# Performance work log

Hardware: AMD Instinct MI355X
Metric: run time of the kernel (lower is better)

Reference implementation:

```python
import jax, jax.numpy as jnp
from jax import lax
import numpy as np

N_FEATURES = 64
B, H, W = 2, 64, 64
EPS = 1e-12  # F.normalize default eps


def setup_inputs() -> dict:
    key = jax.random.key(0)
    ks = jax.random.split(key, 10)
    L = N_FEATURES
    s = 0.02
    return {
        "x": jax.random.normal(ks[0], (B, L, H, W), dtype=jnp.float32),
        "conv1_w": jax.random.normal(ks[1], (L, L, 3, 3), dtype=jnp.float32) * s,
        "conv1_b": jax.random.normal(ks[2], (L,), dtype=jnp.float32) * s,
        "conv2_w": jax.random.normal(ks[3], (L, L, 3, 3), dtype=jnp.float32) * s,
        "conv2_b": jax.random.normal(ks[4], (L,), dtype=jnp.float32) * s,
        "wq": jax.random.normal(ks[5], (L, L), dtype=jnp.float32) * s,
        "wk": jax.random.normal(ks[6], (L, L), dtype=jnp.float32) * s,
        "wv": jax.random.normal(ks[7], (L, L), dtype=jnp.float32) * s,
        "wo": jax.random.normal(ks[8], (L, L), dtype=jnp.float32) * s,
        "bo": jax.random.normal(ks[9], (L,), dtype=jnp.float32) * s,
    }


def _conv3x3(h, w, b):
    y = lax.conv_general_dilated(
        h, w, window_strides=(1, 1), padding=((1, 1), (1, 1)),
        dimension_numbers=("NCHW", "OIHW", "NCHW"))
    return y + b[None, :, None, None]


def _l2norm(a):
    return a / jnp.maximum(jnp.linalg.norm(a, axis=-1, keepdims=True), EPS)


def reference(x, conv1_w, conv1_b, conv2_w, conv2_b, wq, wk, wv, wo, bo):
    # embedding: conv3x3 -> relu -> conv3x3
    h = _conv3x3(x, conv1_w, conv1_b)
    h = jax.nn.relu(h)
    h = _conv3x3(h, conv2_w, conv2_b)  # [B, L, H, W]
    b, l, hh, ww = h.shape
    t = h.reshape(b, l, hh * ww).transpose(0, 2, 1)  # [B, HW, L]
    q = _l2norm(t @ wq.T)  # [B, HW, L]
    k = _l2norm(t @ wk.T)
    v = t @ wv.T
    # per-token rank-1 outer product scores: [B, HW, L, L]
    scores = q[..., :, None] * k[..., None, :]
    p = jax.nn.softmax(scores, axis=-1)
    out = jnp.einsum("bncd,bnd->bnc", p, v)  # [B, HW, L]
    out = out @ wo.T + bo
    out = out.transpose(0, 2, 1).reshape(b, l, hh, ww)
    return out + h
```

## Files before the change

### kernel.cpp

```cpp
#include <hip/hip_runtime.h>
#include <hip/hip_bf16.h>


#define IMG 262144

using frag_ab = __attribute__((ext_vector_type(8))) short;
using frag_cd = __attribute__((ext_vector_type(4))) float;
typedef unsigned u32x4 __attribute__((ext_vector_type(4)));
typedef float    f32x2 __attribute__((ext_vector_type(2)));
typedef float    f32x4 __attribute__((ext_vector_type(4)));

static __device__ inline unsigned short f2bf(float f) {
    unsigned u = __float_as_uint(f);
    return (unsigned short)((u + 0x7FFFu + ((u >> 16) & 1u)) >> 16);
}
static __device__ inline float bflo(unsigned p) { return __uint_as_float(p << 16); }
static __device__ inline float bfhi(unsigned p) { return __uint_as_float(p & 0xFFFF0000u); }

#if __has_builtin(__builtin_amdgcn_fdot2_f32_bf16)
typedef __bf16 bf16x2 __attribute__((ext_vector_type(2)));
static __device__ inline float dot2bf(unsigned a, unsigned b, float c) {
    union U { unsigned u; bf16x2 v; };
    U ua, ub; ua.u = a; ub.u = b;
    return __builtin_amdgcn_fdot2_f32_bf16(ua.v, ub.v, c, false);
}
#else
static __device__ inline float dot2bf(unsigned a, unsigned b, float c) {
    return fmaf(bflo(a), bflo(b), fmaf(bfhi(a), bfhi(b), c));
}
#endif

#if __has_builtin(__builtin_amdgcn_exp2f)
#define EXP2F(x) __builtin_amdgcn_exp2f(x)
#else
#define EXP2F(x) __expf(0.6931471805599453f * (x))
#endif

__global__ __launch_bounds__(256) void prep_w(
    const float* __restrict__ w1, const float* __restrict__ w2,
    const float* __restrict__ wq, const float* __restrict__ wk,
    const float* __restrict__ wv, const float* __restrict__ wo,
    unsigned short* __restrict__ wt1, unsigned short* __restrict__ wt2,
    unsigned* __restrict__ wp)
{
    int i = blockIdx.x * 256 + threadIdx.x;
    if (i < 73728) {
        int mat = i >= 36864;
        int j = i - mat * 36864;
        int tap = j >> 12;
        int oc  = (j >> 6) & 63;
        int ic  = j & 63;
        const float* w = mat ? w2 : w1;
        (mat ? wt2 : wt1)[j] = f2bf(w[(oc * 64 + ic) * 9 + tap]);
    } else {
        int a = i - 73728;
        int mat = a >> 11;
        int r = a & 2047;
        int c = r >> 5, dp = r & 31;
        const float* w = (mat == 0) ? wq : (mat == 1) ? wk : (mat == 2) ? wv : wo;
        unsigned val = (unsigned)f2bf(w[c * 64 + 2 * dp]) |
                       ((unsigned)f2bf(w[c * 64 + 2 * dp + 1]) << 16);
        wp[mat * 2048 + c * 32 + (((dp >> 2) ^ (c & 7)) << 2) + (dp & 3)] = val;
    }
}

__global__ __launch_bounds__(256, 2) void fused_k(
    const float* __restrict__ x,
    const unsigned short* __restrict__ wt1, const unsigned short* __restrict__ wt2,
    const float* __restrict__ b1, const float* __restrict__ b2,
    const unsigned* __restrict__ wp, const float* __restrict__ bo,
    float* __restrict__ out)
{
    __shared__ __align__(16) unsigned       w_lds[6144];
    __shared__ __align__(16) unsigned short xt[5 * 20 * 72];
    __shared__ __align__(16) unsigned short r1[54 * 72];
    __shared__ __align__(16) float          t_lds[16 * 66];
    __shared__ __align__(16) unsigned       tp[16 * 32];
    __shared__ __align__(16) f32x2          kv[8 * 64];
    __shared__ __align__(16) unsigned short o_l[8 * 64];

    const int tid  = threadIdx.x;
    const int b    = blockIdx.x >> 8;
    const int y    = (blockIdx.x >> 2) & 63;
    const int x0   = (blockIdx.x & 3) * 16;
    const int wv_  = tid >> 6;
    const int lane = tid & 63;
    const int m    = lane & 15;
    const int q    = lane >> 4;
    const int oc0  = wv_ * 16;

    frag_ab A1[9][2], A2[9][2];
    #pragma unroll
    for (int t = 0; t < 9; ++t)
        #pragma unroll
        for (int s = 0; s < 2; ++s) {
            A1[t][s] = *(const frag_ab*)&wt1[(t * 64 + oc0 + m) * 64 + s * 32 + q * 8];
            A2[t][s] = *(const frag_ab*)&wt2[(t * 64 + oc0 + m) * 64 + s * 32 + q * 8];
        }

    #pragma unroll
    for (int j = 0; j < 6; ++j)
        ((u32x4*)w_lds)[j * 256 + tid] = ((const u32x4*)wp)[j * 256 + tid];

    {
        const int xl  = tid & 15;
        const int sub = tid >> 4;
        #pragma unroll
        for (int i = 0; i < 20; ++i) {
            int pair = i * 16 + sub;
            int row = pair >> 6, ic = pair & 63;
            int yy = y - 2 + row;
            int yc = min(max(yy, 0), 63);
            float f = x[((b * 64 + ic) * 64 + yc) * 64 + x0 + xl];
            unsigned short v = f2bf(f);
            if (yy != yc) v = 0;
            xt[(row * 20 + xl + 2) * 72 + ic] = v;
        }
        #pragma unroll
        for (int j = 0; j < 5; ++j) {
            int e = j * 256 + tid;
            int col = e & 3, pair = e >> 2;
            int row = pair >> 6, ic = pair & 63;
            int xsl = (col < 2) ? col : col + 16;
            int gx = x0 - 2 + xsl;
            int gxc = min(max(gx, 0), 63);
            int yy = y - 2 + row;
            int yc = min(max(yy, 0), 63);
            float f = x[((b * 64 + ic) * 64 + yc) * 64 + gxc];
            unsigned short v = f2bf(f);
            if (yy != yc || gx != gxc) v = 0;
            xt[(row * 20 + xsl) * 72 + ic] = v;
        }
    }
    __syncthreads();

    int pb[4], rn_[4], xs_[4];
    bool nv[4];
    #pragma unroll
    for (int nt = 0; nt < 4; ++nt) {
        int n  = nt * 16 + m;
        int nc = min(n, 53);
        int rr = nc / 18, xx = nc - rr * 18;
        rn_[nt] = rr; xs_[nt] = xx; nv[nt] = (n < 54);
        pb[nt] = (rr * 20 + xx) * 72 + q * 8;
    }
    frag_cd acc1[4];
    #pragma unroll
    for (int i = 0; i < 4; ++i) acc1[i] = (frag_cd){0.f, 0.f, 0.f, 0.f};

    #pragma unroll
    for (int ky = 0; ky < 3; ++ky)
        #pragma unroll
        for (int kx = 0; kx < 3; ++kx)
            #pragma unroll
            for (int s = 0; s < 2; ++s) {
                frag_ab a = A1[ky * 3 + kx][s];
                int off = (ky * 20 + kx) * 72 + s * 32;
                #pragma unroll
                for (int nt = 0; nt < 4; ++nt)
                    acc1[nt] = __builtin_amdgcn_mfma_f32_16x16x32_bf16(
                        a, *(const frag_ab*)&xt[pb[nt] + off], acc1[nt], 0, 0, 0);
            }

    {
        frag_cd b1f = *(const frag_cd*)&b1[oc0 + q * 4];
        #pragma unroll
        for (int nt = 0; nt < 4; ++nt) {
            if (!nv[nt]) continue;
            int n = nt * 16 + m;
            int gy = y - 1 + rn_[nt];
            int gx = x0 - 1 + xs_[nt];
            bool oob = (gy < 0) | (gy > 63) | (gx < 0) | (gx > 63);
            #pragma unroll
            for (int r = 0; r < 4; ++r) {
                float v = fmaxf(acc1[nt][r] + b1f[r], 0.f);
                r1[n * 72 + oc0 + q * 4 + r] = oob ? (unsigned short)0 : f2bf(v);
            }
        }
    }
    __syncthreads();

    frag_cd acc2 = (frag_cd){0.f, 0.f, 0.f, 0.f};
    #pragma unroll
    for (int ky = 0; ky < 3; ++ky)
        #pragma unroll
        for (int kx = 0; kx < 3; ++kx)
            #pragma unroll
            for (int s = 0; s < 2; ++s)
                acc2 = __builtin_amdgcn_mfma_f32_16x16x32_bf16(
                    A2[ky * 3 + kx][s],
                    *(const frag_ab*)&r1[(ky * 18 + m + kx) * 72 + s * 32 + q * 8],
                    acc2, 0, 0, 0);

    {
        frag_cd b2f = *(const frag_cd*)&b2[oc0 + q * 4];
        float hv[4];
        #pragma unroll
        for (int r = 0; r < 4; ++r) {
            hv[r] = acc2[r] + b2f[r];
            t_lds[m * 66 + oc0 + q * 4 + r] = hv[r];
        }
        int dpb = (oc0 >> 1) + q * 2;
        tp[m * 32 + dpb + 0] = (unsigned)f2bf(hv[0]) | ((unsigned)f2bf(hv[1]) << 16);
        tp[m * 32 + dpb + 1] = (unsigned)f2bf(hv[2]) | ((unsigned)f2bf(hv[3]) << 16);
    }
    __syncthreads();

    const float bo_c = bo[lane];
    const int c7 = lane & 7;
    const unsigned* wop = wp + 6144;
    const int ra_ = wv_ * 2, rb_ = ra_ + 1;

    #pragma unroll
    for (int it = 0; it < 2; ++it) {
        const int ta = wv_ * 4 + it * 2, tb = ta + 1;

        float qa = 0.f, ka = 0.f, va = 0.f, qb = 0.f, kb = 0.f, vb = 0.f;
        #pragma unroll
        for (int dp4 = 0; dp4 < 8; ++dp4) {
            int chunk = ((dp4 ^ c7) << 2);
            u32x4 pq = *(const u32x4*)&w_lds[lane * 32 + chunk];
            u32x4 pk = *(const u32x4*)&w_lds[2048 + lane * 32 + chunk];
            u32x4 pv = *(const u32x4*)&w_lds[4096 + lane * 32 + chunk];
            u32x4 tpa = *(const u32x4*)&tp[ta * 32 + dp4 * 4];
            u32x4 tpb = *(const u32x4*)&tp[tb * 32 + dp4 * 4];
            #pragma unroll
            for (int j = 0; j < 4; ++j) {
                qa = dot2bf(pq[j], tpa[j], qa);
                ka = dot2bf(pk[j], tpa[j], ka);
                va = dot2bf(pv[j], tpa[j], va);
                qb = dot2bf(pq[j], tpb[j], qb);
                kb = dot2bf(pk[j], tpb[j], kb);
                vb = dot2bf(pv[j], tpb[j], vb);
            }
        }

        float nqa = qa * qa, nka = ka * ka, nqb = qb * qb, nkb = kb * kb;
        #pragma unroll
        for (int s = 32; s > 0; s >>= 1) {
            nqa += __shfl_xor(nqa, s);
            nka += __shfl_xor(nka, s);
            nqb += __shfl_xor(nqb, s);
            nkb += __shfl_xor(nkb, s);
        }
        qa = qa / fmaxf(sqrtf(nqa), 1e-12f) * 1.44269504f;
        ka = ka / fmaxf(sqrtf(nka), 1e-12f);
        qb = qb / fmaxf(sqrtf(nqb), 1e-12f) * 1.44269504f;
        kb = kb / fmaxf(sqrtf(nkb), 1e-12f);

        kv[ra_ * 64 + lane] = (f32x2){ka, va};
        kv[rb_ * 64 + lane] = (f32x2){kb, vb};

        float dena = 0.f, numa = 0.f, denb = 0.f, numb = 0.f;
        #pragma unroll 8
        for (int d2 = 0; d2 < 32; ++d2) {
            f32x4 A_ = *(const f32x4*)&kv[ra_ * 64 + d2 * 2];
            f32x4 B_ = *(const f32x4*)&kv[rb_ * 64 + d2 * 2];
            float e0 = EXP2F(qa * A_[0]); dena += e0; numa = fmaf(e0, A_[1], numa);
            float e1 = EXP2F(qa * A_[2]); dena += e1; numa = fmaf(e1, A_[3], numa);
            float e2 = EXP2F(qb * B_[0]); denb += e2; numb = fmaf(e2, B_[1], numb);
            float e3 = EXP2F(qb * B_[2]); denb += e3; numb = fmaf(e3, B_[3], numb);
        }
        float oa = numa / dena, ob = numb / denb;
        o_l[ra_ * 64 + lane] = f2bf(oa);
        o_l[rb_ * 64 + lane] = f2bf(ob);

        float res_a = t_lds[ta * 66 + lane];
        float res_b = t_lds[tb * 66 + lane];
        float oa2 = bo_c, ob2 = bo_c;
        #pragma unroll
        for (int dp4 = 0; dp4 < 8; ++dp4) {
            u32x4 pw  = *(const u32x4*)&wop[lane * 32 + ((dp4 ^ c7) << 2)];
            u32x4 opa = *(const u32x4*)&o_l[ra_ * 64 + dp4 * 8];
            u32x4 opb = *(const u32x4*)&o_l[rb_ * 64 + dp4 * 8];
            #pragma unroll
            for (int j = 0; j < 4; ++j) {
                oa2 = dot2bf(pw[j], opa[j], oa2);
                ob2 = dot2bf(pw[j], opb[j], ob2);
            }
        }
        t_lds[ta * 66 + lane] = oa2 + res_a;
        t_lds[tb * 66 + lane] = ob2 + res_b;
    }
    __syncthreads();

    {
        int c = tid >> 2, xg = tid & 3;
        f32x4 o4;
        #pragma unroll
        for (int j = 0; j < 4; ++j) o4[j] = t_lds[(xg * 4 + j) * 66 + c];
        *(f32x4*)&out[((b * 64 + c) * 64 + y) * 64 + x0 + xg * 4] = o4;
    }
}

extern "C" void kernel_launch(void* const* d_in, const int* in_sizes, int n_in,
                              void* d_out, int out_size, void* d_ws, size_t ws_size,
                              hipStream_t stream) {
    const float* x  = (const float*)d_in[0];
    const float* w1 = (const float*)d_in[1];
    const float* b1 = (const float*)d_in[2];
    const float* w2 = (const float*)d_in[3];
    const float* b2 = (const float*)d_in[4];
    const float* wq = (const float*)d_in[5];
    const float* wk = (const float*)d_in[6];
    const float* wv = (const float*)d_in[7];
    const float* wo = (const float*)d_in[8];
    const float* bo = (const float*)d_in[9];
    float* out = (float*)d_out;

    unsigned*       wpp = (unsigned*)d_ws;
    unsigned short* wt1 = (unsigned short*)((char*)d_ws + 32768);
    unsigned short* wt2 = wt1 + 36864;

    prep_w<<<320, 256, 0, stream>>>(w1, w2, wq, wk, wv, wo, wt1, wt2, wpp);
    fused_k<<<512, 256, 0, stream>>>(x, wt1, wt2, b1, b2, wpp, bo, out);
}
```

Before: 96.88 us.

## Drop weight LDS staging, load fragments coalesced, defer conv2 weights, process four tokens

Weights are repacked so each wave's MFMA A-fragments and the q/k/v/o projection rows load as contiguous coalesced vectors from global memory (L2). The 24KB w_lds staging buffer and its copy are removed. Loading of the conv2 weight fragments is moved until after conv1, which shortens their register lifetime. The occupancy hint is raised from 2 to 3 blocks per CU. The attention stage now handles four tokens per wave in one pass instead of two iterations of two, raising ILP, at the cost of more live registers and of projection weights being read from global/L2 instead of LDS.

```diff
diff --git a/kernel.cpp b/kernel.cpp
--- a/kernel.cpp
+++ b/kernel.cpp
@@ -51,7 +51,10 @@
         int oc  = (j >> 6) & 63;
         int ic  = j & 63;
         const float* w = mat ? w2 : w1;
-        (mat ? wt2 : wt1)[j] = f2bf(w[(oc * 64 + ic) * 9 + tap]);
+        int g = oc >> 4, m = oc & 15;
+        int s = ic >> 5, q = (ic >> 3) & 3, e = ic & 7;
+        int dst = ((((tap * 4 + g) * 2 + s) * 4 + q) * 16 + m) * 8 + e;
+        (mat ? wt2 : wt1)[dst] = f2bf(w[(oc * 64 + ic) * 9 + tap]);
     } else {
         int a = i - 73728;
         int mat = a >> 11;
@@ -60,24 +63,23 @@
         const float* w = (mat == 0) ? wq : (mat == 1) ? wk : (mat == 2) ? wv : wo;
         unsigned val = (unsigned)f2bf(w[c * 64 + 2 * dp]) |
                        ((unsigned)f2bf(w[c * 64 + 2 * dp + 1]) << 16);
-        wp[mat * 2048 + c * 32 + (((dp >> 2) ^ (c & 7)) << 2) + (dp & 3)] = val;
-    }
-}
-
-__global__ __launch_bounds__(256, 2) void fused_k(
+        wp[((mat * 8 + (dp >> 2)) * 64 + c) * 4 + (dp & 3)] = val;
+    }
+}
+
+__global__ __launch_bounds__(256, 3) void fused_k(
     const float* __restrict__ x,
     const unsigned short* __restrict__ wt1, const unsigned short* __restrict__ wt2,
     const float* __restrict__ b1, const float* __restrict__ b2,
     const unsigned* __restrict__ wp, const float* __restrict__ bo,
     float* __restrict__ out)
 {
-    __shared__ __align__(16) unsigned       w_lds[6144];
     __shared__ __align__(16) unsigned short xt[5 * 20 * 72];
     __shared__ __align__(16) unsigned short r1[54 * 72];
     __shared__ __align__(16) float          t_lds[16 * 66];
     __shared__ __align__(16) unsigned       tp[16 * 32];
-    __shared__ __align__(16) f32x2          kv[8 * 64];
-    __shared__ __align__(16) unsigned short o_l[8 * 64];
+    __shared__ __align__(16) f32x2          kv[16 * 64];
+    __shared__ __align__(16) unsigned short o_l[16 * 64];
 
     const int tid  = threadIdx.x;
     const int b    = blockIdx.x >> 8;
@@ -89,18 +91,12 @@
     const int q    = lane >> 4;
     const int oc0  = wv_ * 16;
 
-    frag_ab A1[9][2], A2[9][2];
+    frag_ab A1[9][2];
     #pragma unroll
     for (int t = 0; t < 9; ++t)
         #pragma unroll
-        for (int s = 0; s < 2; ++s) {
-            A1[t][s] = *(const frag_ab*)&wt1[(t * 64 + oc0 + m) * 64 + s * 32 + q * 8];
-            A2[t][s] = *(const frag_ab*)&wt2[(t * 64 + oc0 + m) * 64 + s * 32 + q * 8];
-        }
-
-    #pragma unroll
-    for (int j = 0; j < 6; ++j)
-        ((u32x4*)w_lds)[j * 256 + tid] = ((const u32x4*)wp)[j * 256 + tid];
+        for (int s = 0; s < 2; ++s)
+            A1[t][s] = *(const frag_ab*)&wt1[(((t * 4 + wv_) * 2 + s) * 64 + lane) * 8];
 
     {
         const int xl  = tid & 15;
@@ -162,6 +158,13 @@
                         a, *(const frag_ab*)&xt[pb[nt] + off], acc1[nt], 0, 0, 0);
             }
 
+    frag_ab A2[9][2];
+    #pragma unroll
+    for (int t = 0; t < 9; ++t)
+        #pragma unroll
+        for (int s = 0; s < 2; ++s)
+            A2[t][s] = *(const frag_ab*)&wt2[(((t * 4 + wv_) * 2 + s) * 64 + lane) * 8];
+
     {
         frag_cd b1f = *(const frag_cd*)&b1[oc0 + q * 4];
         #pragma unroll
@@ -207,81 +210,77 @@
     __syncthreads();
 
     const float bo_c = bo[lane];
-    const int c7 = lane & 7;
-    const unsigned* wop = wp + 6144;
-    const int ra_ = wv_ * 2, rb_ = ra_ + 1;
-
-    #pragma unroll
-    for (int it = 0; it < 2; ++it) {
-        const int ta = wv_ * 4 + it * 2, tb = ta + 1;
-
-        float qa = 0.f, ka = 0.f, va = 0.f, qb = 0.f, kb = 0.f, vb = 0.f;
-        #pragma unroll
-        for (int dp4 = 0; dp4 < 8; ++dp4) {
-            int chunk = ((dp4 ^ c7) << 2);
-            u32x4 pq = *(const u32x4*)&w_lds[lane * 32 + chunk];
-            u32x4 pk = *(const u32x4*)&w_lds[2048 + lane * 32 + chunk];
-            u32x4 pv = *(const u32x4*)&w_lds[4096 + lane * 32 + chunk];
-            u32x4 tpa = *(const u32x4*)&tp[ta * 32 + dp4 * 4];
-            u32x4 tpb = *(const u32x4*)&tp[tb * 32 + dp4 * 4];
+    const int t0_ = wv_ * 4;
+
+    float qq[4] = {0,0,0,0}, kk[4] = {0,0,0,0}, vv[4] = {0,0,0,0};
+    #pragma unroll
+    for (int dp4 = 0; dp4 < 8; ++dp4) {
+        u32x4 pq = *(const u32x4*)&wp[(dp4 * 64 + lane) * 4];
+        u32x4 pk = *(const u32x4*)&wp[((8 + dp4) * 64 + lane) * 4];
+        u32x4 pv = *(const u32x4*)&wp[((16 + dp4) * 64 + lane) * 4];
+        #pragma unroll
+        for (int i = 0; i < 4; ++i) {
+            u32x4 tpv = *(const u32x4*)&tp[(t0_ + i) * 32 + dp4 * 4];
             #pragma unroll
             for (int j = 0; j < 4; ++j) {
-                qa = dot2bf(pq[j], tpa[j], qa);
-                ka = dot2bf(pk[j], tpa[j], ka);
-                va = dot2bf(pv[j], tpa[j], va);
-                qb = dot2bf(pq[j], tpb[j], qb);
-                kb = dot2bf(pk[j], tpb[j], kb);
-                vb = dot2bf(pv[j], tpb[j], vb);
+                qq[i] = dot2bf(pq[j], tpv[j], qq[i]);
+                kk[i] = dot2bf(pk[j], tpv[j], kk[i]);
+                vv[i] = dot2bf(pv[j], tpv[j], vv[i]);
             }
         }
-
-        float nqa = qa * qa, nka = ka * ka, nqb = qb * qb, nkb = kb * kb;
-        #pragma unroll
-        for (int s = 32; s > 0; s >>= 1) {
-            nqa += __shfl_xor(nqa, s);
-            nka += __shfl_xor(nka, s);
-            nqb += __shfl_xor(nqb, s);
-            nkb += __shfl_xor(nkb, s);
-        }
-        qa = qa / fmaxf(sqrtf(nqa), 1e-12f) * 1.44269504f;
-        ka = ka / fmaxf(sqrtf(nka), 1e-12f);
-        qb = qb / fmaxf(sqrtf(nqb), 1e-12f) * 1.44269504f;
-        kb = kb / fmaxf(sqrtf(nkb), 1e-12f);
-
-        kv[ra_ * 64 + lane] = (f32x2){ka, va};
-        kv[rb_ * 64 + lane] = (f32x2){kb, vb};
-
-        float dena = 0.f, numa = 0.f, denb = 0.f, numb = 0.f;
-        #pragma unroll 8
-        for (int d2 = 0; d2 < 32; ++d2) {
-            f32x4 A_ = *(const f32x4*)&kv[ra_ * 64 + d2 * 2];
-            f32x4 B_ = *(const f32x4*)&kv[rb_ * 64 + d2 * 2];
-            float e0 = EXP2F(qa * A_[0]); dena += e0; numa = fmaf(e0, A_[1], numa);
-            float e1 = EXP2F(qa * A_[2]); dena += e1; numa = fmaf(e1, A_[3], numa);
-            float e2 = EXP2F(qb * B_[0]); denb += e2; numb = fmaf(e2, B_[1], numb);
-            float e3 = EXP2F(qb * B_[2]); denb += e3; numb = fmaf(e3, B_[3], numb);
-        }
-        float oa = numa / dena, ob = numb / denb;
-        o_l[ra_ * 64 + lane] = f2bf(oa);
-        o_l[rb_ * 64 + lane] = f2bf(ob);
-
-        float res_a = t_lds[ta * 66 + lane];
-        float res_b = t_lds[tb * 66 + lane];
-        float oa2 = bo_c, ob2 = bo_c;
-        #pragma unroll
-        for (int dp4 = 0; dp4 < 8; ++dp4) {
-            u32x4 pw  = *(const u32x4*)&wop[lane * 32 + ((dp4 ^ c7) << 2)];
-            u32x4 opa = *(const u32x4*)&o_l[ra_ * 64 + dp4 * 8];
-            u32x4 opb = *(const u32x4*)&o_l[rb_ * 64 + dp4 * 8];
-            #pragma unroll
-            for (int j = 0; j < 4; ++j) {
-                oa2 = dot2bf(pw[j], opa[j], oa2);
-                ob2 = dot2bf(pw[j], opb[j], ob2);
-            }
-        }
-        t_lds[ta * 66 + lane] = oa2 + res_a;
-        t_lds[tb * 66 + lane] = ob2 + res_b;
-    }
+    }
+
+    float nq[4], nk[4];
+    #pragma unroll
+    for (int i = 0; i < 4; ++i) { nq[i] = qq[i] * qq[i]; nk[i] = kk[i] * kk[i]; }
+    #pragma unroll
+    for (int s = 32; s > 0; s >>= 1)
+        #pragma unroll
+        for (int i = 0; i < 4; ++i) {
+            nq[i] += __shfl_xor(nq[i], s);
+            nk[i] += __shfl_xor(nk[i], s);
+        }
+    #pragma unroll
+    for (int i = 0; i < 4; ++i) {
+        qq[i] = qq[i] / fmaxf(sqrtf(nq[i]), 1e-12f) * 1.44269504f;
+        kk[i] = kk[i] / fmaxf(sqrtf(nk[i]), 1e-12f);
+        kv[(t0_ + i) * 64 + lane] = (f32x2){kk[i], vv[i]};
+    }
+
+    float den[4] = {0,0,0,0}, num[4] = {0,0,0,0};
+    #pragma unroll 4
+    for (int d2 = 0; d2 < 32; ++d2) {
+        #pragma unroll
+        for (int i = 0; i < 4; ++i) {
+            f32x4 K = *(const f32x4*)&kv[(t0_ + i) * 64 + d2 * 2];
+            float e0 = EXP2F(qq[i] * K[0]); den[i] += e0; num[i] = fmaf(e0, K[1], num[i]);
+            float e1 = EXP2F(qq[i] * K[2]); den[i] += e1; num[i] = fmaf(e1, K[3], num[i]);
+        }
+    }
+    #pragma unroll
+    for (int i = 0; i < 4; ++i)
+        o_l[(t0_ + i) * 64 + lane] = f2bf(num[i] / den[i]);
+
+    float res[4], po[4];
+    #pragma unroll
+    for (int i = 0; i < 4; ++i) {
+        res[i] = t_lds[(t0_ + i) * 66 + lane];
+        po[i]  = bo_c;
+    }
+    #pragma unroll
+    for (int dp4 = 0; dp4 < 8; ++dp4) {
+        u32x4 pw = *(const u32x4*)&wp[((24 + dp4) * 64 + lane) * 4];
+        #pragma unroll
+        for (int i = 0; i < 4; ++i) {
+            u32x4 ov = *(const u32x4*)&o_l[(t0_ + i) * 64 + dp4 * 8];
+            #pragma unroll
+            for (int j = 0; j < 4; ++j)
+                po[i] = dot2bf(pw[j], ov[j], po[i]);
+        }
+    }
+    #pragma unroll
+    for (int i = 0; i < 4; ++i)
+        t_lds[(t0_ + i) * 66 + lane] = po[i] + res[i];
     __syncthreads();
 
     {
```

Result: faster. 94.79 us (-2.2%).
